# Optimization experiments

Hardware: AMD Instinct MI355X
Metric: run time of the kernel (lower is better)

The kernel has to match this reference:

```python
import jax, jax.numpy as jnp
import numpy as np
import math
from itertools import combinations_with_replacement

# --- static config matching init_kwargs ---
L = 64          # input_lenght
ORDER = 2       # polynomial order
DIV = 100       # weight_divisor
B = 16384       # batch size

# Precomputed index tuples for combinations-with-replacement of the L inputs.
# Shape: (n_comb, ORDER) with n_comb = C(L+ORDER-1, ORDER) = 2080 for L=64, r=2.
IDX = np.array(list(combinations_with_replacement(range(L), ORDER)), dtype=np.int32)
# Number of weights includes the bias slot: C(L+1+ORDER-1, ORDER) = 2145.
# The original _get_colx only fills the first n_comb columns; the rest stay zero.
NUM_W = math.comb(L + 1 + ORDER - 1, ORDER)


def setup_inputs() -> dict:
    key = jax.random.key(0)
    k1, k2, k3 = jax.random.split(key, 3)
    x = jax.random.normal(k1, (B, L), dtype=jnp.float32)
    W = jax.random.uniform(k2, (NUM_W,), dtype=jnp.float32) / DIV
    b = jax.random.uniform(k3, (1,), dtype=jnp.float32) / DIV
    return {"x": x, "W": W, "b": b}


def reference(x, W, b):
    idx = jnp.asarray(IDX)                      # (n_comb, ORDER)
    # gather + product: colx[i, p] = prod_j x[i, idx[p, j]]
    colx = jnp.prod(x[:, idx], axis=-1)         # (B, n_comb)
    pad = NUM_W - colx.shape[1]                 # trailing zero columns (bias-slot artifact)
    colx = jnp.pad(colx, ((0, 0), (0, pad)))    # (B, NUM_W)
    out = colx @ W.reshape(-1, 1) + b           # (B, 1)
    return out
```

## Files before the change

### kernel.cpp

```cpp
#include <hip/hip_runtime.h>


template <int J0, int J1>
__device__ __forceinline__ void accum_range(const float* __restrict__ W,
                                            const float (&x)[64],
                                            float& acc) {
#pragma unroll
  for (int j = J0; j < J1; ++j) {
    const int base = j * 64 - (j * (j - 1)) / 2;
    float y = 0.0f;
#pragma unroll
    for (int k = j; k < 64; ++k) {
      y = __builtin_fmaf(W[base + (k - j)], x[k], y);
    }
    acc = __builtin_fmaf(x[j], y, acc);
  }
}

__global__ __launch_bounds__(256) void honu_kernel(
    const float* __restrict__ X, const float* __restrict__ W,
    const float* __restrict__ Bias, float* __restrict__ out, int nrows) {
  __shared__ float part[4][64];

  const int tid = threadIdx.x;
  const int lane = tid & 63;
  const int wave = __builtin_amdgcn_readfirstlane(tid >> 6);
  const int row = blockIdx.x * 64 + lane;

  float x[64];
  if (row < nrows) {
    const float4* xp = reinterpret_cast<const float4*>(X + (size_t)row * 64);
#pragma unroll
    for (int q = 0; q < 16; ++q) {
      float4 v = xp[q];
      x[4 * q + 0] = v.x;
      x[4 * q + 1] = v.y;
      x[4 * q + 2] = v.z;
      x[4 * q + 3] = v.w;
    }
  } else {
#pragma unroll
    for (int q = 0; q < 64; ++q) x[q] = 0.0f;
  }

  float acc = 0.0f;
  if (wave == 0) {
    accum_range<0, 8>(W, x, acc);
    accum_range<56, 64>(W, x, acc);
  } else if (wave == 1) {
    accum_range<8, 16>(W, x, acc);
    accum_range<48, 56>(W, x, acc);
  } else if (wave == 2) {
    accum_range<16, 24>(W, x, acc);
    accum_range<40, 48>(W, x, acc);
  } else {
    accum_range<24, 40>(W, x, acc);
  }

  part[wave][lane] = acc;
  __syncthreads();

  if (tid < 64) {
    const int orow = blockIdx.x * 64 + tid;
    if (orow < nrows) {
      float r = part[0][tid] + part[1][tid] + part[2][tid] + part[3][tid] +
                Bias[0];
      out[orow] = r;
    }
  }
}

extern "C" void kernel_launch(void* const* d_in, const int* in_sizes, int n_in,
                              void* d_out, int out_size, void* d_ws,
                              size_t ws_size, hipStream_t stream) {
  const float* X = (const float*)d_in[0];
  const float* W = (const float*)d_in[1];
  const float* Bias = (const float*)d_in[2];
  float* out = (float*)d_out;

  const int nrows = out_size;
  const int grid = (nrows + 63) / 64;
  honu_kernel<<<grid, 256, 0, stream>>>(X, W, Bias, out, nrows);
}
```

Before: 66.36 us.

## Split each row's quadratic form across 16 waves with an LDS-staged x tile

Blocks grow from 256 to 1024 threads, so each 64-row block's work is spread over 16 waves, each handling two mirrored pairs of j indices to balance load. The x tile is loaded once with coalesced float4 reads into padded LDS (stride 65), and each wave reads only the columns it needs into registers. The aim is more waves per row for latency hiding and fewer live registers per thread. In exchange the 16 partial sums go through LDS, adding a larger reduction and an extra barrier, and launch_bounds(1024,4) caps registers.

```diff
diff --git a/kernel.cpp b/kernel.cpp
--- a/kernel.cpp
+++ b/kernel.cpp
@@ -1,5 +1,8 @@
 #include <hip/hip_runtime.h>
 
+
+#define ROWS 64
+#define XSTRIDE 65
 
 template <int J0, int J1>
 __device__ __forceinline__ void accum_range(const float* __restrict__ W,
@@ -17,54 +20,74 @@
   }
 }
 
-__global__ __launch_bounds__(256) void honu_kernel(
+template <int S>
+__device__ __forceinline__ float wave_work(const float* __restrict__ W,
+                                           const float* __restrict__ xrow) {
+  float x[64];
+#pragma unroll
+  for (int k = 2 * S; k < 64; ++k) x[k] = xrow[k];
+  float acc = 0.0f;
+  accum_range<2 * S, 2 * S + 2>(W, x, acc);
+  accum_range<62 - 2 * S, 64 - 2 * S>(W, x, acc);
+  return acc;
+}
+
+__global__ __launch_bounds__(1024, 4) void honu_kernel(
     const float* __restrict__ X, const float* __restrict__ W,
     const float* __restrict__ Bias, float* __restrict__ out, int nrows) {
-  __shared__ float part[4][64];
+  __shared__ float tile[ROWS * XSTRIDE];
+  __shared__ float part[16][64];
 
   const int tid = threadIdx.x;
   const int lane = tid & 63;
-  const int wave = __builtin_amdgcn_readfirstlane(tid >> 6);
-  const int row = blockIdx.x * 64 + lane;
+  const int wave = tid >> 6;
+  const int row0 = blockIdx.x * ROWS;
 
-  float x[64];
-  if (row < nrows) {
-    const float4* xp = reinterpret_cast<const float4*>(X + (size_t)row * 64);
-#pragma unroll
-    for (int q = 0; q < 16; ++q) {
-      float4 v = xp[q];
-      x[4 * q + 0] = v.x;
-      x[4 * q + 1] = v.y;
-      x[4 * q + 2] = v.z;
-      x[4 * q + 3] = v.w;
+  {
+    const int r = tid >> 4;
+    const int c = (tid & 15) << 2;
+    float4 v = make_float4(0.f, 0.f, 0.f, 0.f);
+    if (row0 + r < nrows) {
+      v = reinterpret_cast<const float4*>(X)[(size_t)(row0 + r) * 16 +
+                                             (tid & 15)];
     }
-  } else {
-#pragma unroll
-    for (int q = 0; q < 64; ++q) x[q] = 0.0f;
+    float* dst = &tile[r * XSTRIDE + c];
+    dst[0] = v.x;
+    dst[1] = v.y;
+    dst[2] = v.z;
+    dst[3] = v.w;
   }
+  __syncthreads();
 
+  const float* xrow = &tile[lane * XSTRIDE];
   float acc = 0.0f;
-  if (wave == 0) {
-    accum_range<0, 8>(W, x, acc);
-    accum_range<56, 64>(W, x, acc);
-  } else if (wave == 1) {
-    accum_range<8, 16>(W, x, acc);
-    accum_range<48, 56>(W, x, acc);
-  } else if (wave == 2) {
-    accum_range<16, 24>(W, x, acc);
-    accum_range<40, 48>(W, x, acc);
-  } else {
-    accum_range<24, 40>(W, x, acc);
+  switch (wave) {
+    case 0:  acc = wave_work<0>(W, xrow);  break;
+    case 1:  acc = wave_work<1>(W, xrow);  break;
+    case 2:  acc = wave_work<2>(W, xrow);  break;
+    case 3:  acc = wave_work<3>(W, xrow);  break;
+    case 4:  acc = wave_work<4>(W, xrow);  break;
+    case 5:  acc = wave_work<5>(W, xrow);  break;
+    case 6:  acc = wave_work<6>(W, xrow);  break;
+    case 7:  acc = wave_work<7>(W, xrow);  break;
+    case 8:  acc = wave_work<8>(W, xrow);  break;
+    case 9:  acc = wave_work<9>(W, xrow);  break;
+    case 10: acc = wave_work<10>(W, xrow); break;
+    case 11: acc = wave_work<11>(W, xrow); break;
+    case 12: acc = wave_work<12>(W, xrow); break;
+    case 13: acc = wave_work<13>(W, xrow); break;
+    case 14: acc = wave_work<14>(W, xrow); break;
+    default: acc = wave_work<15>(W, xrow); break;
   }
-
   part[wave][lane] = acc;
   __syncthreads();
 
   if (tid < 64) {
-    const int orow = blockIdx.x * 64 + tid;
+    const int orow = row0 + tid;
     if (orow < nrows) {
-      float r = part[0][tid] + part[1][tid] + part[2][tid] + part[3][tid] +
-                Bias[0];
+      float r = Bias[0];
+#pragma unroll
+      for (int w = 0; w < 16; ++w) r += part[w][tid];
       out[orow] = r;
     }
   }
@@ -79,6 +102,6 @@
   float* out = (float*)d_out;
 
   const int nrows = out_size;
-  const int grid = (nrows + 63) / 64;
-  honu_kernel<<<grid, 256, 0, stream>>>(X, W, Bias, out, nrows);
+  const int grid = (nrows + ROWS - 1) / ROWS;
+  honu_kernel<<<grid, 1024, 0, stream>>>(X, W, Bias, out, nrows);
 }
```

New measurement: 60.08 us. 1.1x faster.
